# Kernel optimization log

Measured on AMD Instinct MI355X. Metric: run time of the kernel, lower is better.

Reference implementation:

```python
import jax, jax.numpy as jnp
import numpy as np

BATCH, IN, HID, OUT = 8192, 1024, 4096, 1000

def _l2norm_rows(w):
    # matches F.normalize(p=2, dim=1) with eps=1e-12
    n = jnp.linalg.norm(w, axis=1, keepdims=True)
    return w / jnp.maximum(n, 1e-12)

def setup_inputs() -> dict:
    key = jax.random.key(0)
    k1, k2, k3 = jax.random.split(key, 3)
    x = jax.random.normal(k1, (BATCH, IN), dtype=jnp.float32)
    kohonen_w = _l2norm_rows(jax.random.normal(k2, (HID, IN), dtype=jnp.float32))
    grossberg_w = _l2norm_rows(jax.random.normal(k3, (OUT, HID), dtype=jnp.float32))
    return {"x": x, "kohonen_w": kohonen_w, "grossberg_w": grossberg_w}

def reference(x, kohonen_w, grossberg_w):
    # x: [B, D]; kohonen_w: [H, D]; grossberg_w: [O, H]
    x2 = jnp.sum(x * x, axis=1, keepdims=True)            # [B, 1]
    w2 = jnp.sum(kohonen_w * kohonen_w, axis=1)           # [H]
    d2 = x2 - 2.0 * (x @ kohonen_w.T) + w2[None, :]       # [B, H]
    winners = jnp.argmin(d2, axis=1)                      # [B] (argmin of dist == argmin of dist^2)
    # one-hot @ grossberg_w.T is exactly a row gather of grossberg_w.T
    output = grossberg_w.T[winners]                       # [B, O]
    return output, winners, x.shape[0]
```

## Files before the change

kernel.cpp:

```cpp
#include <hip/hip_runtime.h>
#include <stdint.h>

#define B_SZ 8192
#define D_SZ 1024
#define H_SZ 4096
#define O_SZ 1000

#define MARGIN 0.0625f

typedef float f32x4 __attribute__((ext_vector_type(4)));
typedef __bf16 bf16x8 __attribute__((ext_vector_type(8)));

static __device__ __forceinline__ uint16_t f2bf(float f) {
  uint32_t u = __float_as_uint(f);
  uint32_t r = (u + 0x7fffu + ((u >> 16) & 1u)) >> 16;
  return (uint16_t)r;
}

__global__ __launch_bounds__(256) void prep(const float* __restrict__ x,
                                            uint16_t* __restrict__ xb,
                                            const float* __restrict__ w,
                                            uint16_t* __restrict__ wb,
                                            double* __restrict__ w2d) {
  const int bid = blockIdx.x;
  const int tid = threadIdx.x;
  if (bid < 8192) {
    const int i = bid * 256 + tid;
    f32x4 v = reinterpret_cast<const f32x4*>(x)[i];
    ushort4 o;
    o.x = f2bf(v[0]); o.y = f2bf(v[1]); o.z = f2bf(v[2]); o.w = f2bf(v[3]);
    reinterpret_cast<ushort4*>(xb)[i] = o;
  } else {
    const int h = (bid - 8192) * 4 + (tid >> 6);
    const int l = tid & 63;
    const f32x4* wr = reinterpret_cast<const f32x4*>(w + (size_t)h * D_SZ);
    ushort4* wo = reinterpret_cast<ushort4*>(wb + (size_t)h * D_SZ);
    double s = 0.0;
#pragma unroll
    for (int j = 0; j < 4; ++j) {
      f32x4 v = wr[j * 64 + l];
      s += (double)v[0] * v[0] + (double)v[1] * v[1] + (double)v[2] * v[2] + (double)v[3] * v[3];
      ushort4 o;
      o.x = f2bf(v[0]); o.y = f2bf(v[1]); o.z = f2bf(v[2]); o.w = f2bf(v[3]);
      wo[j * 64 + l] = o;
    }
#pragma unroll
    for (int m = 32; m; m >>= 1) s += __shfl_xor(s, m);
    if (l == 0) w2d[h] = s;
  }
}

__global__ __launch_bounds__(512, 2) void kohonen_gemm256(const uint16_t* __restrict__ xb,
                                                          const uint16_t* __restrict__ wb,
                                                          float* __restrict__ tmax64,
                                                          unsigned long long* __restrict__ tmask64) {
  extern __shared__ char smem[];
  const int tid = threadIdx.x;
  const int lane = tid & 63, wid = tid >> 6;
  const int wm = wid >> 2, wn = wid & 3;
  const int r15 = lane & 15, g = lane >> 4;
  const int xorv = (r15 & 7) << 4;
  const int lr = lane >> 3, lp = lane & 7;

  const int bid = blockIdx.x;
  const int wg = (bid & 7) * 64 + (bid >> 3);
  const int bm = wg >> 4, bn = wg & 15;

  const uint16_t* xrow = xb + (size_t)(bm * 256) * D_SZ;
  const uint16_t* wrow = wb + (size_t)(bn * 256) * D_SZ;

  f32x4 acc[8][4] = {};
  bf16x8 Af[4][2];
  bf16x8 Bf[2][2][2];

  auto stage_a = [&](int a, int sp, int kt) {
#pragma unroll
    for (int j = 0; j < 2; ++j) {
      const int pp = lp ^ lr;
      const int sr = wid * 16 + j * 8 + lr;
      const int mr = (sr < 64) ? (a * 64 + sr) : (128 + a * 64 + (sr - 64));
      const uint16_t* src = xrow + (size_t)mr * D_SZ + kt * 64 + pp * 8;
      __builtin_amdgcn_global_load_lds(
          (const __attribute__((address_space(1))) uint32_t*)src,
          (__attribute__((address_space(3))) uint32_t*)(smem + (sp * 2 + a) * 16384 +
                                                        (wid * 16 + j * 8) * 128),
          16, 0, 0);
    }
  };
  auto stage_b = [&](int b, int sp, int kt) {
#pragma unroll
    for (int j = 0; j < 2; ++j) {
      const int pp = lp ^ lr;
      const int sr = wid * 16 + j * 8 + lr;
      const int mr = (sr >> 5) * 64 + b * 32 + (sr & 31);
      const uint16_t* src = wrow + (size_t)mr * D_SZ + kt * 64 + pp * 8;
      __builtin_amdgcn_global_load_lds(
          (const __attribute__((address_space(1))) uint32_t*)src,
          (__attribute__((address_space(3))) uint32_t*)(smem + 65536 + (sp * 2 + b) * 16384 +
                                                        (wid * 16 + j * 8) * 128),
          16, 0, 0);
    }
  };

#define LDA(QM)                                                                  \
  {                                                                              \
    const char* Abq = smem + rp * 32768 + (QM)*16384;                            \
    _Pragma("unroll") for (int mi = 0; mi < 4; ++mi) {                           \
      const int sr = wm * 64 + mi * 16 + r15;                                    \
      _Pragma("unroll") for (int ks = 0; ks < 2; ++ks)                           \
          Af[mi][ks] = *reinterpret_cast<const bf16x8*>(                         \
              Abq + ((sr * 128 + ks * 64 + g * 16) ^ xorv));                     \
    }                                                                            \
  }
#define LDB(QN)                                                                  \
  {                                                                              \
    const char* Bbq = smem + 65536 + rp * 32768 + (QN)*16384;                    \
    _Pragma("unroll") for (int ni = 0; ni < 2; ++ni) {                           \
      const int sr = wn * 32 + ni * 16 + r15;                                    \
      _Pragma("unroll") for (int ks = 0; ks < 2; ++ks)                           \
          Bf[QN][ni][ks] = *reinterpret_cast<const bf16x8*>(                     \
              Bbq + ((sr * 128 + ks * 64 + g * 16) ^ xorv));                     \
    }                                                                            \
  }
#define MFMAQ(QM, QN)                                                            \
  __builtin_amdgcn_s_setprio(1);                                                 \
  _Pragma("unroll") for (int mi = 0; mi < 4; ++mi)                               \
      _Pragma("unroll") for (int ni = 0; ni < 2; ++ni)                           \
          _Pragma("unroll") for (int ks = 0; ks < 2; ++ks)                       \
              acc[(QM)*4 + mi][(QN)*2 + ni] = __builtin_amdgcn_mfma_f32_16x16x32_bf16( \
                  Af[mi][ks], Bf[QN][ni][ks], acc[(QM)*4 + mi][(QN)*2 + ni], 0, 0, 0); \
  __builtin_amdgcn_s_setprio(0);

  stage_a(0, 0, 0);
  stage_b(0, 0, 0);
  stage_b(1, 0, 0);
  stage_a(1, 0, 0);

  for (int t = 0; t < 16; ++t) {
    const int rp = t & 1, sp = rp ^ 1, kt = t + 1;
    const bool pf = (t < 15);
    asm volatile("s_waitcnt vmcnt(0)" ::: "memory");
    __builtin_amdgcn_s_barrier();
    LDA(0);
    LDB(0);
    if (pf) stage_a(0, sp, kt);
    MFMAQ(0, 0);
    LDB(1);
    if (pf) stage_b(0, sp, kt);
    MFMAQ(0, 1);
    LDA(1);
    if (pf) stage_b(1, sp, kt);
    MFMAQ(1, 1);
    if (pf) stage_a(1, sp, kt);
    MFMAQ(1, 0);
  }

  const int tile = bn * 4 + wn;
#pragma unroll
  for (int m = 0; m < 8; ++m) {
    float v[4];
#pragma unroll
    for (int j = 0; j < 4; ++j)
      v[j] = fmaxf(fmaxf(acc[m][0][j], acc[m][1][j]), fmaxf(acc[m][2][j], acc[m][3][j]));
#pragma unroll
    for (int s = 1; s < 16; s <<= 1) {
#pragma unroll
      for (int j = 0; j < 4; ++j) v[j] = fmaxf(v[j], __shfl_xor(v[j], s));
    }
    unsigned long long mk[4];
#pragma unroll
    for (int j = 0; j < 4; ++j) {
      unsigned long long bmask = 0;
      const float thr = v[j] - MARGIN;
#pragma unroll
      for (int n = 0; n < 4; ++n)
        if (acc[m][n][j] >= thr) bmask |= 1ull << (n * 16 + r15);
      mk[j] = bmask;
    }
#pragma unroll
    for (int s = 1; s < 16; s <<= 1) {
#pragma unroll
      for (int j = 0; j < 4; ++j) mk[j] |= __shfl_xor(mk[j], s);
    }
    if (r15 == 0) {
#pragma unroll
      for (int j = 0; j < 4; ++j) {
        const int row = bm * 256 + wm * 128 + m * 16 + g * 4 + j;
        tmax64[(size_t)row * 64 + tile] = v[j];
        tmask64[(size_t)row * 64 + tile] = mk[j];
      }
    }
  }
}

__global__ __launch_bounds__(64) void rescore_gather(const float* __restrict__ x,
                                                     const float* __restrict__ w,
                                                     const double* __restrict__ w2d,
                                                     const float* __restrict__ tmax64,
                                                     const unsigned long long* __restrict__ tmask64,
                                                     const float* __restrict__ gt,
                                                     float* __restrict__ out,
                                                     float* __restrict__ winners_f) {
  const int row = blockIdx.x;
  const int l = threadIdx.x;

  f32x4 xr[4];
  const f32x4* xp = reinterpret_cast<const f32x4*>(x + (size_t)row * D_SZ);
#pragma unroll
  for (int j = 0; j < 4; ++j) xr[j] = xp[j * 64 + l];

  const float pmax = tmax64[(size_t)row * 64 + l];
  const unsigned long long pmask = tmask64[(size_t)row * 64 + l];
  float M = pmax;
#pragma unroll
  for (int m = 1; m < 64; m <<= 1) M = fmaxf(M, __shfl_xor(M, m));
  const float thr = M - MARGIN;

  double bestS = -1e300;
  int bestI = 0x7fffffff;

  unsigned long long bits = __ballot(pmax >= thr && pmask != 0ull);
  while (bits) {
    const int src = __ffsll(bits) - 1;
    unsigned long long tmask = __shfl(pmask, src);
    const int tile = src;
    while (tmask) {
      const int b = __ffsll(tmask) - 1;
      const int h = tile * 64 + b;
      const f32x4* wp = reinterpret_cast<const f32x4*>(w + (size_t)h * D_SZ);
      double dot = 0.0;
#pragma unroll
      for (int j = 0; j < 4; ++j) {
        f32x4 wv = wp[j * 64 + l];
        dot += (double)xr[j][0] * wv[0] + (double)xr[j][1] * wv[1] +
               (double)xr[j][2] * wv[2] + (double)xr[j][3] * wv[3];
      }
#pragma unroll
      for (int m = 32; m; m >>= 1) dot += __shfl_xor(dot, m);
      const double sc = 2.0 * dot - w2d[h];
      if (sc > bestS || (sc == bestS && h < bestI)) { bestS = sc; bestI = h; }
      tmask &= tmask - 1;
    }
    bits &= bits - 1;
  }

  if (l == 0) winners_f[row] = (float)bestI;
  const f32x4* gsrc = reinterpret_cast<const f32x4*>(gt + (size_t)bestI * O_SZ);
  f32x4* gdst = reinterpret_cast<f32x4*>(out + (size_t)row * O_SZ);
  for (int i = l; i < O_SZ / 4; i += 64) gdst[i] = gsrc[i];
  if (row == 0 && l == 0)
    out[(size_t)B_SZ * O_SZ + B_SZ] = (float)B_SZ;
}

__global__ __launch_bounds__(256) void transpose_g(const float* __restrict__ g,
                                                   float* __restrict__ gt) {
  __shared__ float t[32][33];
  const int h0 = blockIdx.x * 32;
  const int o0 = blockIdx.y * 32;
  const int lx = threadIdx.x & 31, ly = threadIdx.x >> 5;
  for (int i = ly; i < 32; i += 8) {
    const int o = o0 + i;
    t[i][lx] = (o < O_SZ) ? g[(size_t)o * H_SZ + (h0 + lx)] : 0.f;
  }
  __syncthreads();
  for (int i = ly; i < 32; i += 8) {
    const int o = o0 + lx;
    if (o < O_SZ) gt[(size_t)(h0 + i) * O_SZ + o] = t[lx][i];
  }
}

extern "C" void kernel_launch(void* const* d_in, const int* in_sizes, int n_in,
                              void* d_out, int out_size, void* d_ws, size_t ws_size,
                              hipStream_t stream) {
  const float* x  = (const float*)d_in[0];
  const float* kw = (const float*)d_in[1];
  const float* gw = (const float*)d_in[2];
  float* out = (float*)d_out;
  char* ws = (char*)d_ws;

  uint16_t*           xb   = (uint16_t*)(ws);
  uint16_t*           wb   = (uint16_t*)(ws + 16777216);
  float*              tmx  = (float*)   (ws + 25165824);
  unsigned long long* tmk  = (unsigned long long*)(ws + 27262976);
  double*             w2d  = (double*)  (ws + 31457280);
  float*              gt   = (float*)   (ws);

  prep<<<9216, 256, 0, stream>>>(x, xb, kw, wb, w2d);

  static bool attr_set = false;
  if (!attr_set) {
    hipFuncSetAttribute((const void*)kohonen_gemm256,
                        hipFuncAttributeMaxDynamicSharedMemorySize, 131072);
    attr_set = true;
  }
  kohonen_gemm256<<<512, 512, 131072, stream>>>(xb, wb, tmx, tmk);

  dim3 g3(H_SZ / 32, (O_SZ + 31) / 32);
  transpose_g<<<g3, 256, 0, stream>>>(gw, gt);

  rescore_gather<<<B_SZ, 64, 0, stream>>>(x, kw, w2d, tmx, tmk, gt, out,
                                          out + (size_t)B_SZ * O_SZ);
}
```

Measured before the change: 118.0 us.

## Use per-quarter vmcnt waits and barriers instead of full drain per k-tile

Replaces the single vmcnt(0)+barrier at the top of each k-tile with finer-grained vmcnt(4) waits and barriers after each of the four staged quarter loads. Each LDS quarter only has to land before the step that reads it, so global-to-LDS loads overlap more with MFMA work. The loop is also unrolled by two so the read-buffer index is a compile-time constant. The cost is four barriers per k-tile instead of one, and correctness now depends on the vmcnt counts matching the issue order exactly.

Result: slower. 132.5 us (+12.3%).

```diff
diff --git a/kernel.cpp b/kernel.cpp
--- a/kernel.cpp
+++ b/kernel.cpp
@@ -102,9 +102,9 @@
     }
   };
 
-#define LDA(QM)                                                                  \
+#define LDA(RP, QM)                                                              \
   {                                                                              \
-    const char* Abq = smem + rp * 32768 + (QM)*16384;                            \
+    const char* Abq = smem + (RP)*32768 + (QM)*16384;                            \
     _Pragma("unroll") for (int mi = 0; mi < 4; ++mi) {                           \
       const int sr = wm * 64 + mi * 16 + r15;                                    \
       _Pragma("unroll") for (int ks = 0; ks < 2; ++ks)                           \
@@ -112,9 +112,9 @@
               Abq + ((sr * 128 + ks * 64 + g * 16) ^ xorv));                     \
     }                                                                            \
   }
-#define LDB(QN)                                                                  \
+#define LDB(RP, QN)                                                              \
   {                                                                              \
-    const char* Bbq = smem + 65536 + rp * 32768 + (QN)*16384;                    \
+    const char* Bbq = smem + 65536 + (RP)*32768 + (QN)*16384;                    \
     _Pragma("unroll") for (int ni = 0; ni < 2; ++ni) {                           \
       const int sr = wn * 32 + ni * 16 + r15;                                    \
       _Pragma("unroll") for (int ks = 0; ks < 2; ++ks)                           \
@@ -131,28 +131,53 @@
                   Af[mi][ks], Bf[QN][ni][ks], acc[(QM)*4 + mi][(QN)*2 + ni], 0, 0, 0); \
   __builtin_amdgcn_s_setprio(0);
 
+#define KTILE(T, RP)                                                             \
+  {                                                                              \
+    const int kt_ = (T) + 1;                                                     \
+    const int sp_ = (RP) ^ 1;                                                    \
+    const bool pf_ = ((T) < 15);                                                 \
+    LDA(RP, 0);                                                                  \
+    LDB(RP, 0);                                                                  \
+    if (pf_) {                                                                   \
+      stage_a(0, sp_, kt_);                                                      \
+      asm volatile("s_waitcnt vmcnt(4)" ::: "memory");                           \
+    } else {                                                                     \
+      asm volatile("s_waitcnt vmcnt(0)" ::: "memory");                           \
+    }                                                                            \
+    __builtin_amdgcn_s_barrier();                                                \
+    MFMAQ(0, 0);                                                                 \
+    LDB(RP, 1);                                                                  \
+    if (pf_) {                                                                   \
+      stage_b(0, sp_, kt_);                                                      \
+      asm volatile("s_waitcnt vmcnt(4)" ::: "memory");                           \
+    }                                                                            \
+    __builtin_amdgcn_s_barrier();                                                \
+    MFMAQ(0, 1);                                                                 \
+    LDA(RP, 1);                                                                  \
+    if (pf_) {                                                                   \
+      stage_b(1, sp_, kt_);                                                      \
+      asm volatile("s_waitcnt vmcnt(4)" ::: "memory");                           \
+    }                                                                            \
+    __builtin_amdgcn_s_barrier();                                                \
+    MFMAQ(1, 1);                                                                 \
+    if (pf_) {                                                                   \
+      stage_a(1, sp_, kt_);                                                      \
+      asm volatile("s_waitcnt vmcnt(4)" ::: "memory");                           \
+    }                                                                            \
+    __builtin_amdgcn_s_barrier();                                                \
+    MFMAQ(1, 0);                                                                 \
+  }
+
   stage_a(0, 0, 0);
   stage_b(0, 0, 0);
   stage_b(1, 0, 0);
   stage_a(1, 0, 0);
-
-  for (int t = 0; t < 16; ++t) {
-    const int rp = t & 1, sp = rp ^ 1, kt = t + 1;
-    const bool pf = (t < 15);
-    asm volatile("s_waitcnt vmcnt(0)" ::: "memory");
-    __builtin_amdgcn_s_barrier();
-    LDA(0);
-    LDB(0);
-    if (pf) stage_a(0, sp, kt);
-    MFMAQ(0, 0);
-    LDB(1);
-    if (pf) stage_b(0, sp, kt);
-    MFMAQ(0, 1);
-    LDA(1);
-    if (pf) stage_b(1, sp, kt);
-    MFMAQ(1, 1);
-    if (pf) stage_a(1, sp, kt);
-    MFMAQ(1, 0);
+  asm volatile("s_waitcnt vmcnt(4)" ::: "memory");
+  __builtin_amdgcn_s_barrier();
+
+  for (int tt = 0; tt < 8; ++tt) {
+    KTILE(2 * tt, 0);
+    KTILE(2 * tt + 1, 1);
   }
 
   const int tile = bn * 4 + wn;
```
